# Performance work log

Measured on AMD Instinct MI355X. Metric: run time of the kernel, lower is better.

The kernel has to match this reference:

```python
import jax, jax.numpy as jnp
import numpy as np


def setup_inputs() -> dict:
    key = jax.random.key(0)
    k1, k2 = jax.random.split(key)
    preds = jax.random.normal(k1, (16, 4096, 3), dtype=jnp.float32)
    gts = jax.random.normal(k2, (16, 4096, 3), dtype=jnp.float32)
    return {"preds": preds, "gts": gts}


def _pairwise_sqdist(x, y):
    # x: [B, N1, D], y: [B, N2, D] -> P: [B, N1, N2]
    rx = jnp.sum(x * x, axis=-1)  # [B, N1]
    ry = jnp.sum(y * y, axis=-1)  # [B, N2]
    zz = jnp.einsum("bnd,bmd->bnm", x, y)  # [B, N1, N2]
    return rx[:, :, None] + ry[:, None, :] - 2.0 * zz


def reference(preds, gts):
    # Symmetric Hausdorff distance (squared-dist version) per batch element.
    P = _pairwise_sqdist(preds, gts)  # [B, N1, N2]
    # min over preds (axis 1) for each gt point, then max over gt points
    loss1 = jnp.max(jnp.min(P, axis=1), axis=1)  # [B]
    # min over gts (axis 2) for each pred point, then max over pred points
    loss2 = jnp.max(jnp.min(P, axis=2), axis=1)  # [B]
    return (loss1 + loss2) * 0.5
```

## Files before the change

### kernel.cpp

```cpp
#include <hip/hip_runtime.h>
#include <math.h>


#define NPTS 4096
#define NB 16
#define TPB 256
#define WAVES 4
#define HPW 64
#define HPB (WAVES * HPW)
#define NHB (NPTS / HPB)
#define SPLIT 2
#define OPP (NPTS / SPLIT)
#define TILES (OPP / 32)

#define WSMIN_N (2 * NB * NPTS)

typedef _Float16 h8 __attribute__((ext_vector_type(8)));
typedef float f16v __attribute__((ext_vector_type(16)));

template <int CTRL>
__device__ __forceinline__ float min_dpp(float v) {
    int s = __builtin_amdgcn_update_dpp(0, __float_as_int(v), CTRL, 0xF, 0xF, true);
    return fminf(v, __int_as_float(s));
}

__global__ __launch_bounds__(TPB) void haus_scan_kernel(
        const float* __restrict__ preds, const float* __restrict__ gts,
        unsigned int* __restrict__ wsmin) {
    const int hb  = blockIdx.x & (NHB - 1);
    const int sp  = blockIdx.x >> 4;
    const int b   = blockIdx.y;
    const int dir = blockIdx.z;
    const int t   = threadIdx.x;
    const int lane = t & 63, w = t >> 6;
    const int l31 = lane & 31, half = lane >> 5;

    const float* home = (dir == 0) ? gts : preds;
    const float* opp  = (dir == 0) ? preds : gts;
    const float* hbp = home + (size_t)b * NPTS * 3;
    const float* obp = opp  + (size_t)b * NPTS * 3;

    __shared__ h8 srec[2 * OPP];
    __shared__ float shg[WAVES][HPW];

    for (int i = 0; i < OPP / TPB; ++i) {
        int p = i * TPB + t;
        const float* s = obp + (size_t)(sp * OPP + p) * 3;
        float x = s[0], y = s[1], z = s[2];
        float hp = fmaf(x, x, fmaf(y, y, z * z));
        _Float16 xh = (_Float16)x, yh = (_Float16)y, zh = (_Float16)z;
        _Float16 xl = (_Float16)(x - (float)xh);
        _Float16 yl = (_Float16)(y - (float)yh);
        _Float16 zl = (_Float16)(z - (float)zh);
        _Float16 hph = (_Float16)hp, hpl = (_Float16)(hp - (float)hph);
        h8 lo, hi;
        lo[0] = xh; lo[1] = yh; lo[2] = zh;
        lo[3] = xl; lo[4] = yl; lo[5] = zl;
        lo[6] = xh; lo[7] = yh;
        hi[0] = zh;
        hi[1] = hph; hi[2] = hpl;
        hi[3] = (_Float16)0; hi[4] = (_Float16)0;
        hi[5] = (_Float16)0; hi[6] = (_Float16)0; hi[7] = (_Float16)0;
        srec[p] = lo;
        srec[OPP + p] = hi;
    }

    h8 afrag[2];
#pragma unroll
    for (int a = 0; a < 2; ++a) {
        int m = hb * HPB + w * HPW + a * 32 + l31;
        float gx = hbp[m * 3 + 0], gy = hbp[m * 3 + 1], gz = hbp[m * 3 + 2];
        float hg = fmaf(gx, gx, fmaf(gy, gy, gz * gz));
        shg[w][a * 32 + l31] = hg;
        _Float16 gxh = (_Float16)gx, gyh = (_Float16)gy, gzh = (_Float16)gz;
        _Float16 gxl = (_Float16)(gx - (float)gxh);
        _Float16 gyl = (_Float16)(gy - (float)gyh);
        _Float16 gzl = (_Float16)(gz - (float)gzh);
        const _Float16 n2 = (_Float16)(-2.0f);
        h8 f;
        if (half == 0) {
            f[0] = n2 * gxh; f[1] = n2 * gyh; f[2] = n2 * gzh;
            f[3] = n2 * gxh; f[4] = n2 * gyh; f[5] = n2 * gzh;
            f[6] = n2 * gxl; f[7] = n2 * gyl;
        } else {
            f[0] = n2 * gzl;
            f[1] = (_Float16)1; f[2] = (_Float16)1;
            f[3] = (_Float16)0; f[4] = (_Float16)0;
            f[5] = (_Float16)0; f[6] = (_Float16)0; f[7] = (_Float16)0;
        }
        afrag[a] = f;
    }

    f16v zc = {};
    float best0[16], best1[16];
#pragma unroll
    for (int r = 0; r < 16; ++r) { best0[r] = INFINITY; best1[r] = INFINITY; }

    __syncthreads();

    const int base = half * OPP + l31;
#pragma unroll 2
    for (int tt = 0; tt < TILES; ++tt) {
        h8 bfrag = srec[base + tt * 32];
        f16v D0 = __builtin_amdgcn_mfma_f32_32x32x16_f16(afrag[0], bfrag, zc, 0, 0, 0);
        f16v D1 = __builtin_amdgcn_mfma_f32_32x32x16_f16(afrag[1], bfrag, zc, 0, 0, 0);
#pragma unroll
        for (int r = 0; r < 16; ++r) best0[r] = fminf(best0[r], D0[r]);
#pragma unroll
        for (int r = 0; r < 16; ++r) best1[r] = fminf(best1[r], D1[r]);
    }

#pragma unroll
    for (int r = 0; r < 16; ++r) {
        float a0 = best0[r], a1 = best1[r];
        a0 = min_dpp<0x121>(a0); a1 = min_dpp<0x121>(a1);
        a0 = min_dpp<0x122>(a0); a1 = min_dpp<0x122>(a1);
        a0 = min_dpp<0x124>(a0); a1 = min_dpp<0x124>(a1);
        a0 = min_dpp<0x128>(a0); a1 = min_dpp<0x128>(a1);
        float s0 = __int_as_float(__builtin_amdgcn_ds_swizzle(__float_as_int(a0), 0x401F));
        float s1 = __int_as_float(__builtin_amdgcn_ds_swizzle(__float_as_int(a1), 0x401F));
        best0[r] = fminf(a0, s0);
        best1[r] = fminf(a1, s1);
    }

    unsigned int* slot = wsmin + ((size_t)dir * NB + b) * NPTS + hb * HPB + w * HPW;
    if (l31 == 0) {
#pragma unroll
        for (int r = 0; r < 16; ++r) {
            int row = (r & 3) + 8 * (r >> 2) + 4 * half;
            float d0 = fmaxf(best0[r] + shg[w][row], 0.0f);
            float d1 = fmaxf(best1[r] + shg[w][32 + row], 0.0f);
            atomicMin(slot + row, __float_as_uint(d0));
            atomicMin(slot + 32 + row, __float_as_uint(d1));
        }
    }
}

__global__ __launch_bounds__(TPB) void haus_final_kernel(
        const unsigned int* __restrict__ wsmin, float* __restrict__ out) {
    const int b = blockIdx.x;
    const int t = threadIdx.x;
    const float4* w0 = (const float4*)(wsmin + ((size_t)0 * NB + b) * NPTS);
    const float4* w1 = (const float4*)(wsmin + ((size_t)1 * NB + b) * NPTS);
    float m1 = -INFINITY, m2 = -INFINITY;
#pragma unroll
    for (int r = 0; r < NPTS / 4 / TPB; ++r) {
        float4 a = w0[r * TPB + t];
        float4 c = w1[r * TPB + t];
        m1 = fmaxf(fmaxf(fmaxf(a.x, a.y), fmaxf(a.z, a.w)), m1);
        m2 = fmaxf(fmaxf(fmaxf(c.x, c.y), fmaxf(c.z, c.w)), m2);
    }
#pragma unroll
    for (int off = 32; off > 0; off >>= 1) {
        m1 = fmaxf(m1, __shfl_down(m1, off, 64));
        m2 = fmaxf(m2, __shfl_down(m2, off, 64));
    }
    __shared__ float s1[4], s2[4];
    if ((t & 63) == 0) { s1[t >> 6] = m1; s2[t >> 6] = m2; }
    __syncthreads();
    if (t == 0) {
        float a = fmaxf(fmaxf(s1[0], s1[1]), fmaxf(s1[2], s1[3]));
        float c = fmaxf(fmaxf(s2[0], s2[1]), fmaxf(s2[2], s2[3]));
        out[b] = 0.5f * (a + c);
    }
}

extern "C" void kernel_launch(void* const* d_in, const int* in_sizes, int n_in,
                              void* d_out, int out_size, void* d_ws, size_t ws_size,
                              hipStream_t stream) {
    const float* preds = (const float*)d_in[0];
    const float* gts   = (const float*)d_in[1];
    float* out = (float*)d_out;
    unsigned int* wsmin = (unsigned int*)d_ws;

    hipMemsetAsync(wsmin, 0xFF, (size_t)WSMIN_N * sizeof(unsigned int), stream);

    haus_scan_kernel<<<dim3(NHB * SPLIT, NB, 2), dim3(TPB), 0, stream>>>(
        preds, gts, wsmin);

    haus_final_kernel<<<dim3(NB), dim3(TPB), 0, stream>>>(wsmin, out);
}
```

Before: 89.80 us.

## Compute both Hausdorff directions from one distance matrix pass

Drops the second grid dimension that recomputed the transposed distance matrix. Each block now computes full squared distances inside the MFMA, with the home norm folded into the A fragment and a ones column in B. It derives row minima as before and column minima by reducing each tile across the wave, using LDS atomics followed by global atomics. SPLIT rises to 4 so the block count stays the same. This halves the MFMA work, but every tile now pays an extra 32-element min reduction, a cross-half shuffle and LDS atomics.

```diff
diff --git a/kernel.cpp b/kernel.cpp
--- a/kernel.cpp
+++ b/kernel.cpp
@@ -6,10 +6,10 @@
 #define NB 16
 #define TPB 256
 #define WAVES 4
-#define HPW 64
-#define HPB (WAVES * HPW)
-#define NHB (NPTS / HPB)
-#define SPLIT 2
+#define GPW 64
+#define GPB (WAVES * GPW)
+#define NGB (NPTS / GPB)
+#define SPLIT 4
 #define OPP (NPTS / SPLIT)
 #define TILES (OPP / 32)
 
@@ -27,25 +27,23 @@
 __global__ __launch_bounds__(TPB) void haus_scan_kernel(
         const float* __restrict__ preds, const float* __restrict__ gts,
         unsigned int* __restrict__ wsmin) {
-    const int hb  = blockIdx.x & (NHB - 1);
+    const int gt  = blockIdx.x & (NGB - 1);
     const int sp  = blockIdx.x >> 4;
     const int b   = blockIdx.y;
-    const int dir = blockIdx.z;
     const int t   = threadIdx.x;
     const int lane = t & 63, w = t >> 6;
     const int l31 = lane & 31, half = lane >> 5;
 
-    const float* home = (dir == 0) ? gts : preds;
-    const float* opp  = (dir == 0) ? preds : gts;
-    const float* hbp = home + (size_t)b * NPTS * 3;
-    const float* obp = opp  + (size_t)b * NPTS * 3;
+    const float* gbp = gts   + (size_t)b * NPTS * 3;
+    const float* pbp = preds + (size_t)b * NPTS * 3;
 
     __shared__ h8 srec[2 * OPP];
-    __shared__ float shg[WAVES][HPW];
+    __shared__ int scol[OPP];
 
+#pragma unroll
     for (int i = 0; i < OPP / TPB; ++i) {
         int p = i * TPB + t;
-        const float* s = obp + (size_t)(sp * OPP + p) * 3;
+        const float* s = pbp + (size_t)(sp * OPP + p) * 3;
         float x = s[0], y = s[1], z = s[2];
         float hp = fmaf(x, x, fmaf(y, y, z * z));
         _Float16 xh = (_Float16)x, yh = (_Float16)y, zh = (_Float16)z;
@@ -59,23 +57,24 @@
         lo[6] = xh; lo[7] = yh;
         hi[0] = zh;
         hi[1] = hph; hi[2] = hpl;
-        hi[3] = (_Float16)0; hi[4] = (_Float16)0;
+        hi[3] = (_Float16)1; hi[4] = (_Float16)1;
         hi[5] = (_Float16)0; hi[6] = (_Float16)0; hi[7] = (_Float16)0;
         srec[p] = lo;
         srec[OPP + p] = hi;
+        scol[p] = 0x7F800000;
     }
 
     h8 afrag[2];
 #pragma unroll
     for (int a = 0; a < 2; ++a) {
-        int m = hb * HPB + w * HPW + a * 32 + l31;
-        float gx = hbp[m * 3 + 0], gy = hbp[m * 3 + 1], gz = hbp[m * 3 + 2];
+        int m = gt * GPB + w * GPW + a * 32 + l31;
+        float gx = gbp[m * 3 + 0], gy = gbp[m * 3 + 1], gz = gbp[m * 3 + 2];
         float hg = fmaf(gx, gx, fmaf(gy, gy, gz * gz));
-        shg[w][a * 32 + l31] = hg;
         _Float16 gxh = (_Float16)gx, gyh = (_Float16)gy, gzh = (_Float16)gz;
         _Float16 gxl = (_Float16)(gx - (float)gxh);
         _Float16 gyl = (_Float16)(gy - (float)gyh);
         _Float16 gzl = (_Float16)(gz - (float)gzh);
+        _Float16 hgh = (_Float16)hg, hgl = (_Float16)(hg - (float)hgh);
         const _Float16 n2 = (_Float16)(-2.0f);
         h8 f;
         if (half == 0) {
@@ -85,7 +84,7 @@
         } else {
             f[0] = n2 * gzl;
             f[1] = (_Float16)1; f[2] = (_Float16)1;
-            f[3] = (_Float16)0; f[4] = (_Float16)0;
+            f[3] = hgh; f[4] = hgl;
             f[5] = (_Float16)0; f[6] = (_Float16)0; f[7] = (_Float16)0;
         }
         afrag[a] = f;
@@ -98,16 +97,23 @@
 
     __syncthreads();
 
-    const int base = half * OPP + l31;
+    const h8* sptr = srec + half * OPP + l31;
 #pragma unroll 2
     for (int tt = 0; tt < TILES; ++tt) {
-        h8 bfrag = srec[base + tt * 32];
+        h8 bfrag = sptr[tt * 32];
         f16v D0 = __builtin_amdgcn_mfma_f32_32x32x16_f16(afrag[0], bfrag, zc, 0, 0, 0);
         f16v D1 = __builtin_amdgcn_mfma_f32_32x32x16_f16(afrag[1], bfrag, zc, 0, 0, 0);
 #pragma unroll
         for (int r = 0; r < 16; ++r) best0[r] = fminf(best0[r], D0[r]);
 #pragma unroll
         for (int r = 0; r < 16; ++r) best1[r] = fminf(best1[r], D1[r]);
+        float cm = fminf(D0[0], D1[0]);
+#pragma unroll
+        for (int r = 1; r < 16; ++r)
+            cm = fminf(fminf(cm, D0[r]), D1[r]);
+        cm = fminf(cm, __shfl_xor(cm, 32, 64));
+        if (half == 0)
+            atomicMin(&scol[tt * 32 + l31], __float_as_int(cm));
     }
 
 #pragma unroll
@@ -122,17 +128,25 @@
         best0[r] = fminf(a0, s0);
         best1[r] = fminf(a1, s1);
     }
-
-    unsigned int* slot = wsmin + ((size_t)dir * NB + b) * NPTS + hb * HPB + w * HPW;
+    unsigned int* wsrow = wsmin + ((size_t)0 * NB + b) * NPTS + gt * GPB + w * GPW;
     if (l31 == 0) {
 #pragma unroll
         for (int r = 0; r < 16; ++r) {
             int row = (r & 3) + 8 * (r >> 2) + 4 * half;
-            float d0 = fmaxf(best0[r] + shg[w][row], 0.0f);
-            float d1 = fmaxf(best1[r] + shg[w][32 + row], 0.0f);
-            atomicMin(slot + row, __float_as_uint(d0));
-            atomicMin(slot + 32 + row, __float_as_uint(d1));
+            float d0 = fmaxf(best0[r], 0.0f);
+            float d1 = fmaxf(best1[r], 0.0f);
+            atomicMin(wsrow + row, __float_as_uint(d0));
+            atomicMin(wsrow + 32 + row, __float_as_uint(d1));
         }
+    }
+
+    __syncthreads();
+    unsigned int* wscol = wsmin + ((size_t)1 * NB + b) * NPTS + sp * OPP;
+#pragma unroll
+    for (int i = 0; i < OPP / TPB; ++i) {
+        int p = i * TPB + t;
+        float c = fmaxf(__int_as_float(scol[p]), 0.0f);
+        atomicMin(wscol + p, __float_as_uint(c));
     }
 }
 
@@ -175,7 +189,7 @@
 
     hipMemsetAsync(wsmin, 0xFF, (size_t)WSMIN_N * sizeof(unsigned int), stream);
 
-    haus_scan_kernel<<<dim3(NHB * SPLIT, NB, 2), dim3(TPB), 0, stream>>>(
+    haus_scan_kernel<<<dim3(NGB * SPLIT, NB, 1), dim3(TPB), 0, stream>>>(
         preds, gts, wsmin);
 
     haus_final_kernel<<<dim3(NB), dim3(TPB), 0, stream>>>(wsmin, out);
```

New measurement: 85.31 us. 5.0% less time.
